# Kernel tuning notes

Measured on AMD Instinct MI355X. Metric: run time of the kernel, lower is better.

Reference implementation:

```python
import jax, jax.numpy as jnp
import numpy as np

DX, DZ, DT = 10.0, 10.0, 1.0e-3
NX, NZ = 512, 512
NSTEPS, NREC = 512, 128
DT2 = DT * DT
INV_DXDZ = 1.0 / (DX * DZ)


def setup_inputs() -> dict:
    key = jax.random.key(0)
    k1, k2, k3, k4 = jax.random.split(key, 4)
    # velocity in [1500, 2500] m/s -> CFL stable with dt=1e-3, dx=dz=10
    velocity_model = 1500.0 + 1000.0 * jax.random.uniform(k1, (NX, NZ), dtype=jnp.float32)
    source = jax.random.normal(k2, (NSTEPS,), dtype=jnp.float32)
    rec_x = jax.random.randint(k3, (NREC,), 0, NX)
    rec_z = jax.random.randint(k4, (NREC,), 0, NZ)
    return {
        "velocity_model": velocity_model,
        "source": source,
        "src_x": 256,
        "src_z": 8,
        "rec_x": rec_x,
        "rec_z": rec_z,
    }


def _laplacian(p):
    # 3x3 cross stencil with zero padding, scaled by 1/(dx*dz) -- identical to
    # F.conv2d(p, [[0,1,0],[1,-4,1],[0,1,0]]/(dx*dz), padding=1)
    pp = jnp.pad(p, 1)
    return (pp[:-2, 1:-1] + pp[2:, 1:-1] + pp[1:-1, :-2] + pp[1:-1, 2:] - 4.0 * p) * INV_DXDZ


def reference(velocity_model, source, src_x, src_z, rec_x, rec_z):
    v2_dt2 = velocity_model * velocity_model * DT2  # [nx, nz]

    def step(carry, s_t):
        p, p_old = carry
        p_new = 2.0 * p - p_old + v2_dt2 * _laplacian(p)
        p_new = p_new.at[src_x, src_z].add(s_t * DT2)
        return (p_new, p), p_new[rec_x, rec_z]  # gather all receivers at once

    p0 = jnp.zeros((NX, NZ), dtype=velocity_model.dtype)
    _, recs = jax.lax.scan(step, (p0, p0), source)  # recs: [n_steps, n_rec]
    return recs.T  # seismogram: [n_rec, n_steps]
```

## Files before the change

### kernel.cpp

```cpp
#include <hip/hip_runtime.h>


#define NXd 512
#define NZd 512
#define NSTEPSd 512
#define NRECd 128
#define DT2f 1.0e-6f
#define INVf 1.0e-2f
#define TBk 16
#define TIk 32
#define EXTk 64
#define NTILEk 16
#define PADk 16
#define PWk 544
#define LROWS 66
#define NROUNDS (NSTEPSd / TBk)

__device__ __forceinline__ float dpp_shr1(float x) {
    int v = __builtin_amdgcn_update_dpp(0, __builtin_bit_cast(int, x),
                                        0x138, 0xF, 0xF, false);
    return __builtin_bit_cast(float, v);
}
__device__ __forceinline__ float dpp_shl1(float x) {
    int v = __builtin_amdgcn_update_dpp(0, __builtin_bit_cast(int, x),
                                        0x130, 0xF, 0xF, false);
    return __builtin_bit_cast(float, v);
}

__device__ __forceinline__ float2 ldg_f2(const float2* p) {
    unsigned long long v = __hip_atomic_load(
        (const unsigned long long*)p, __ATOMIC_RELAXED, __HIP_MEMORY_SCOPE_AGENT);
    return __builtin_bit_cast(float2, v);
}
__device__ __forceinline__ void stg_f2(float2* p, float2 x) {
    __hip_atomic_store((unsigned long long*)p,
                       __builtin_bit_cast(unsigned long long, x),
                       __ATOMIC_RELAXED, __HIP_MEMORY_SCOPE_AGENT);
}

__global__ __launch_bounds__(1024) void fdtd_persist(
    const float* __restrict__ vel, const float* __restrict__ source,
    const int* __restrict__ src_x, const int* __restrict__ src_z,
    const int* __restrict__ rec_x, const int* __restrict__ rec_z,
    float2* __restrict__ PA, float2* __restrict__ PB,
    float* __restrict__ out, unsigned* __restrict__ done)
{
    __shared__ float sb[2][LROWS * EXTk];

    const int tid = threadIdx.x;
    const int w   = tid >> 6;
    const int ez  = tid & 63;
    const int bx = blockIdx.x, by = blockIdx.y;
    const int gx0 = by * TIk;
    const int gz0 = bx * TIk;
    const int ox = gx0 - TBk, oz = gz0 - TBk;
    const int myid = (by * NTILEk + bx) * 32;

    for (int i = tid; i < 34 * 34; i += 1024) {
        const int p = (by * 34 + i / 34) * PWk + (bx * 34 + i % 34);
        stg_f2(&PA[p], make_float2(0.f, 0.f));
        stg_f2(&PB[p], make_float2(0.f, 0.f));
    }

    bool rOwn = false; int rIdx = 0;
    if (tid < NRECd) {
        const int rx = rec_x[tid], rz = rec_z[tid];
        rOwn = (rx >= gx0 && rx < gx0 + TIk && rz >= gz0 && rz < gz0 + TIk);
        rIdx = (rx - ox + 1) * EXTk + (rz - oz);
        if (rOwn) {
            float4* o4 = (float4*)&out[tid * NSTEPSd];
            #pragma unroll
            for (int j = 0; j < NSTEPSd / 4; ++j) o4[j] = make_float4(0.f, 0.f, 0.f, 0.f);
        }
    }

    float rV2i[4];
    {
        const int fz = oz + ez;
        #pragma unroll
        for (int i = 0; i < 4; ++i) {
            const int fx = ox + 4 * w + i;
            float v2 = 0.f;
            if (fx >= 0 && fx < NXd && fz >= 0 && fz < NZd) {
                float v = vel[fx * NZd + fz];
                v2 = v * v * (DT2f * INVf);
            }
            rV2i[i] = v2;
        }
    }

    if (w == 0) {
        sb[0][ez] = 0.f;
        sb[0][(LROWS - 1) * EXTk + ez] = 0.f;
        sb[1][ez] = 0.f;
        sb[1][(LROWS - 1) * EXTk + ez] = 0.f;
    }

    const int sx = *src_x, sz = *src_z;
    const int exs = sx - ox, ezs = sz - oz;
    const bool srcHere = (exs >= 0 && exs < EXTk && ezs >= 0 && ezs < EXTk) &&
                         (tid == (((exs >> 2) << 6) | ezs));

    const int dxm = max(0, max(ox - sx, sx - (ox + EXTk - 1)));
    const int dzm = max(0, max(oz - sz, sz - (oz + EXTk - 1)));
    const int dman = dxm + dzm;
    const int kAct = dman <= (TBk + 1) ? 0 : (dman - (TBk + 1) + TBk - 1) / TBk;

    int nb = myid;
    if (tid < 8) {
        const int d = (tid < 4) ? tid : tid + 1;
        const int ny = min(NTILEk - 1, max(0, by + d / 3 - 1));
        const int nx = min(NTILEk - 1, max(0, bx + d % 3 - 1));
        nb = (ny * NTILEk + nx) * 32;
    }

    const int pbase = (gx0 + 4 * w) * PWk + gz0 + ez;
    const int fbase = 4 * w * EXTk + ez;

    __syncthreads();
    if (tid == 0)
        __hip_atomic_store(&done[myid], (unsigned)(kAct + 1),
                           __ATOMIC_RELAXED, __HIP_MEMORY_SCOPE_AGENT);

    for (int k = kAct; k < NROUNDS; ++k) {
        const int t0 = TBk * k;

        if (tid < 8) {
            const unsigned tgt = (unsigned)(k + 1);
            while (__hip_atomic_load(&done[nb], __ATOMIC_RELAXED,
                                     __HIP_MEMORY_SCOPE_AGENT) < tgt)
                __builtin_amdgcn_s_sleep(1);
        }
        __syncthreads();

        float2* __restrict__ Pin  = (k & 1) ? PB : PA;
        float2* __restrict__ Pout = (k & 1) ? PA : PB;

        float2 co[4];
        #pragma unroll
        for (int i = 0; i < 4; ++i) co[i] = ldg_f2(&Pin[pbase + i * PWk]);

        float rCur[4], rOld[4];
        #pragma unroll
        for (int i = 0; i < 4; ++i) {
            rCur[i] = co[i].x; rOld[i] = co[i].y;
            sb[0][(4 * w + 1 + i) * EXTk + ez] = rCur[i];
        }

        float sv[TBk];
        if (srcHere) {
            #pragma unroll
            for (int s = 0; s < TBk; ++s) sv[s] = source[t0 + s] * DT2f;
        }

        __syncthreads();

        float rv[TBk];
        #pragma unroll
        for (int s = 0; s < TBk; ++s) {
            const float* cur = sb[s & 1];
            float* nxt = sb[(s & 1) ^ 1];
            const float up0 = cur[fbase];
            const float dn3 = cur[fbase + 5 * EXTk];
            float nv[4];
            #pragma unroll
            for (int i = 0; i < 4; ++i) {
                const float up = (i == 0) ? up0 : rCur[i - 1];
                const float dn = (i == 3) ? dn3 : rCur[i + 1];
                const float lf = dpp_shr1(rCur[i]);
                const float rt = dpp_shl1(rCur[i]);
                const float sum = (up + dn) + (lf + rt);
                const float t4 = __builtin_fmaf(-4.0f, rCur[i], sum);
                const float pm = __builtin_fmaf(2.0f, rCur[i], -rOld[i]);
                nv[i] = __builtin_fmaf(rV2i[i], t4, pm);
            }
            #pragma unroll
            for (int i = 0; i < 4; ++i) {
                rOld[i] = rCur[i];
                rCur[i] = nv[i];
                nxt[fbase + (1 + i) * EXTk] = nv[i];
            }
            if (srcHere) {
                #pragma unroll
                for (int i = 0; i < 4; ++i) {
                    if (i == (exs & 3)) {
                        rCur[i] += sv[s];
                        nxt[(exs + 1) * EXTk + ezs] = rCur[i];
                    }
                }
            }
            __syncthreads();
            if (rOwn) rv[s] = nxt[rIdx];
        }

        if (w >= 4 && w < 12 && ez >= TBk && ez < EXTk - TBk) {
            #pragma unroll
            for (int i = 0; i < 4; ++i)
                stg_f2(&Pout[pbase + i * PWk], make_float2(rCur[i], rOld[i]));
        }

        if (rOwn) {
            #pragma unroll
            for (int s = 0; s < TBk; ++s)
                out[tid * NSTEPSd + t0 + s] = rv[s];
        }

        __syncthreads();
        if (tid == 0)
            __hip_atomic_store(&done[myid], (unsigned)(k + 2),
                               __ATOMIC_RELAXED, __HIP_MEMORY_SCOPE_AGENT);
    }
}

extern "C" void kernel_launch(void* const* d_in, const int* in_sizes, int n_in,
                              void* d_out, int out_size, void* d_ws, size_t ws_size,
                              hipStream_t stream) {
    const float* vel    = (const float*)d_in[0];
    const float* source = (const float*)d_in[1];
    const int*   src_x  = (const int*)d_in[2];
    const int*   src_z  = (const int*)d_in[3];
    const int*   rec_x  = (const int*)d_in[4];
    const int*   rec_z  = (const int*)d_in[5];
    float* out = (float*)d_out;

    const size_t FP = (size_t)PWk * PWk;
    float2* PA = (float2*)d_ws;
    float2* PB = PA + FP;
    unsigned* DONE = (unsigned*)(PB + FP);

    hipMemsetAsync(DONE, 0, (size_t)NTILEk * NTILEk * 32 * sizeof(unsigned), stream);

    void* args[] = {(void*)&vel, (void*)&source, (void*)&src_x, (void*)&src_z,
                    (void*)&rec_x, (void*)&rec_z, (void*)&PA, (void*)&PB,
                    (void*)&out, (void*)&DONE};
    hipLaunchCooperativeKernel((void*)fdtd_persist, dim3(NTILEk, NTILEk),
                               dim3(1024), args, 0, stream);
}
```

Baseline: 340.0 us.

## Compute two timesteps per LDS exchange with redundant halo rows to halve barriers

Each wave now reads two halo rows on each side (stored as float2 cur/old pairs) and computes two timesteps per group, recomputing the extra halo rows redundantly. This halves the number of __syncthreads and LDS exchanges per round, from 16 to 8. In exchange each group adds about 50% more stencil arithmetic, wider LDS traffic (float2) and more registers. Source injection and receiver sampling are adapted to handle the pair of steps.

```diff
diff --git a/kernel.cpp b/kernel.cpp
--- a/kernel.cpp
+++ b/kernel.cpp
@@ -13,8 +13,9 @@
 #define NTILEk 16
 #define PADk 16
 #define PWk 544
-#define LROWS 66
+#define LROWS 68
 #define NROUNDS (NSTEPSd / TBk)
+#define NGRP 8
 
 __device__ __forceinline__ float dpp_shr1(float x) {
     int v = __builtin_amdgcn_update_dpp(0, __builtin_bit_cast(int, x),
@@ -45,7 +46,7 @@
     float2* __restrict__ PA, float2* __restrict__ PB,
     float* __restrict__ out, unsigned* __restrict__ done)
 {
-    __shared__ float sb[2][LROWS * EXTk];
+    __shared__ float2 sb[2][LROWS * EXTk];
 
     const int tid = threadIdx.x;
     const int w   = tid >> 6;
@@ -66,7 +67,7 @@
     if (tid < NRECd) {
         const int rx = rec_x[tid], rz = rec_z[tid];
         rOwn = (rx >= gx0 && rx < gx0 + TIk && rz >= gz0 && rz < gz0 + TIk);
-        rIdx = (rx - ox + 1) * EXTk + (rz - oz);
+        rIdx = (rx - ox + 2) * EXTk + (rz - oz);
         if (rOwn) {
             float4* o4 = (float4*)&out[tid * NSTEPSd];
             #pragma unroll
@@ -74,32 +75,35 @@
         }
     }
 
-    float rV2i[4];
+    float rV2x[6];
     {
         const int fz = oz + ez;
         #pragma unroll
-        for (int i = 0; i < 4; ++i) {
-            const int fx = ox + 4 * w + i;
+        for (int j = 0; j < 6; ++j) {
+            const int fx = ox + 4 * w - 1 + j;
             float v2 = 0.f;
             if (fx >= 0 && fx < NXd && fz >= 0 && fz < NZd) {
                 float v = vel[fx * NZd + fz];
                 v2 = v * v * (DT2f * INVf);
             }
-            rV2i[i] = v2;
+            rV2x[j] = v2;
         }
     }
 
     if (w == 0) {
-        sb[0][ez] = 0.f;
-        sb[0][(LROWS - 1) * EXTk + ez] = 0.f;
-        sb[1][ez] = 0.f;
-        sb[1][(LROWS - 1) * EXTk + ez] = 0.f;
+        #pragma unroll
+        for (int b = 0; b < 2; ++b) {
+            sb[b][0 * EXTk + ez]  = make_float2(0.f, 0.f);
+            sb[b][1 * EXTk + ez]  = make_float2(0.f, 0.f);
+            sb[b][66 * EXTk + ez] = make_float2(0.f, 0.f);
+            sb[b][67 * EXTk + ez] = make_float2(0.f, 0.f);
+        }
     }
 
     const int sx = *src_x, sz = *src_z;
     const int exs = sx - ox, ezs = sz - oz;
-    const bool srcHere = (exs >= 0 && exs < EXTk && ezs >= 0 && ezs < EXTk) &&
-                         (tid == (((exs >> 2) << 6) | ezs));
+    const int jA0 = exs - (4 * w - 1);
+    const bool svTouch = (ez == ezs) && (jA0 >= 0) && (jA0 < 6);
 
     const int dxm = max(0, max(ox - sx, sx - (ox + EXTk - 1)));
     const int dzm = max(0, max(oz - sz, sz - (oz + EXTk - 1)));
@@ -115,7 +119,7 @@
     }
 
     const int pbase = (gx0 + 4 * w) * PWk + gz0 + ez;
-    const int fbase = 4 * w * EXTk + ez;
+    const int rd0 = (4 * w) * EXTk + ez;
 
     __syncthreads();
     if (tid == 0)
@@ -144,11 +148,11 @@
         #pragma unroll
         for (int i = 0; i < 4; ++i) {
             rCur[i] = co[i].x; rOld[i] = co[i].y;
-            sb[0][(4 * w + 1 + i) * EXTk + ez] = rCur[i];
+            sb[0][(4 * w + 2 + i) * EXTk + ez] = co[i];
         }
 
         float sv[TBk];
-        if (srcHere) {
+        if (svTouch) {
             #pragma unroll
             for (int s = 0; s < TBk; ++s) sv[s] = source[t0 + s] * DT2f;
         }
@@ -157,40 +161,53 @@
 
         float rv[TBk];
         #pragma unroll
-        for (int s = 0; s < TBk; ++s) {
-            const float* cur = sb[s & 1];
-            float* nxt = sb[(s & 1) ^ 1];
-            const float up0 = cur[fbase];
-            const float dn3 = cur[fbase + 5 * EXTk];
-            float nv[4];
+        for (int g = 0; g < NGRP; ++g) {
+            const float2* cur = sb[g & 1];
+            float2* nxt = sb[(g & 1) ^ 1];
+            const float2 h0 = cur[rd0];
+            const float2 h1 = cur[rd0 + EXTk];
+            const float2 h4 = cur[rd0 + 6 * EXTk];
+            const float2 h5 = cur[rd0 + 7 * EXTk];
+            const float curv[8] = {h0.x, h1.x, rCur[0], rCur[1],
+                                   rCur[2], rCur[3], h4.x, h5.x};
+            const float oldA[6] = {h1.y, rOld[0], rOld[1],
+                                   rOld[2], rOld[3], h4.y};
+            float cA[6];
+            #pragma unroll
+            for (int j = 0; j < 6; ++j) {
+                const float c = curv[j + 1];
+                const float sum = (curv[j] + curv[j + 2]) +
+                                  (dpp_shr1(c) + dpp_shl1(c));
+                cA[j] = __builtin_fmaf(rV2x[j], __builtin_fmaf(-4.0f, c, sum),
+                                       __builtin_fmaf(2.0f, c, -oldA[j]));
+            }
+            #pragma unroll
+            for (int j = 0; j < 6; ++j)
+                if (j == jA0 && svTouch) cA[j] += sv[2 * g];
+            float cB[4];
             #pragma unroll
             for (int i = 0; i < 4; ++i) {
-                const float up = (i == 0) ? up0 : rCur[i - 1];
-                const float dn = (i == 3) ? dn3 : rCur[i + 1];
-                const float lf = dpp_shr1(rCur[i]);
-                const float rt = dpp_shl1(rCur[i]);
-                const float sum = (up + dn) + (lf + rt);
-                const float t4 = __builtin_fmaf(-4.0f, rCur[i], sum);
-                const float pm = __builtin_fmaf(2.0f, rCur[i], -rOld[i]);
-                nv[i] = __builtin_fmaf(rV2i[i], t4, pm);
-            }
+                const float c = cA[i + 1];
+                const float sum = (cA[i] + cA[i + 2]) +
+                                  (dpp_shr1(c) + dpp_shl1(c));
+                cB[i] = __builtin_fmaf(rV2x[i + 1], __builtin_fmaf(-4.0f, c, sum),
+                                       __builtin_fmaf(2.0f, c, -rCur[i]));
+            }
+            #pragma unroll
+            for (int i = 0; i < 4; ++i)
+                if (i + 1 == jA0 && svTouch) cB[i] += sv[2 * g + 1];
             #pragma unroll
             for (int i = 0; i < 4; ++i) {
-                rOld[i] = rCur[i];
-                rCur[i] = nv[i];
-                nxt[fbase + (1 + i) * EXTk] = nv[i];
-            }
-            if (srcHere) {
-                #pragma unroll
-                for (int i = 0; i < 4; ++i) {
-                    if (i == (exs & 3)) {
-                        rCur[i] += sv[s];
-                        nxt[(exs + 1) * EXTk + ezs] = rCur[i];
-                    }
-                }
+                rOld[i] = cA[i + 1];
+                rCur[i] = cB[i];
+                nxt[(4 * w + 2 + i) * EXTk + ez] = make_float2(cB[i], cA[i + 1]);
             }
             __syncthreads();
-            if (rOwn) rv[s] = nxt[rIdx];
+            if (rOwn) {
+                const float2 rr = nxt[rIdx];
+                rv[2 * g]     = rr.y;
+                rv[2 * g + 1] = rr.x;
+            }
         }
 
         if (w >= 4 && w < 12 && ez >= TBk && ez < EXTk - TBk) {
```

Result: slower. 382.5 us (+12.5%).

## Poll neighbor flags per wave and drop LDS staging barriers at round start

Applied to the files above, without the earlier changes.

Every wavefront now spins on the eight neighbor-tile done flags itself, so the block-wide barrier after polling goes away. The initial LDS write of the tile plus its barrier is also removed: step 0 takes its vertical halo directly from global memory, and the workspace is shifted by one padded row so the row above the tile stays in bounds. The tile's done flag is now published before the receiver samples are written to the output, and the polling sleep grows longer when a neighbor is more than one round behind. Together these shorten the inter-tile dependency chain per time block, in exchange for more global polling traffic and subtler memory-ordering assumptions.

```diff
diff --git a/kernel.cpp b/kernel.cpp
--- a/kernel.cpp
+++ b/kernel.cpp
@@ -32,6 +32,11 @@
         (const unsigned long long*)p, __ATOMIC_RELAXED, __HIP_MEMORY_SCOPE_AGENT);
     return __builtin_bit_cast(float2, v);
 }
+__device__ __forceinline__ float ldg_f1(const float* p) {
+    unsigned v = __hip_atomic_load(
+        (const unsigned*)p, __ATOMIC_RELAXED, __HIP_MEMORY_SCOPE_AGENT);
+    return __builtin_bit_cast(float, v);
+}
 __device__ __forceinline__ void stg_f2(float2* p, float2 x) {
     __hip_atomic_store((unsigned long long*)p,
                        __builtin_bit_cast(unsigned long long, x),
@@ -106,9 +111,10 @@
     const int dman = dxm + dzm;
     const int kAct = dman <= (TBk + 1) ? 0 : (dman - (TBk + 1) + TBk - 1) / TBk;
 
+    const int lane = tid & 63;
     int nb = myid;
-    if (tid < 8) {
-        const int d = (tid < 4) ? tid : tid + 1;
+    if (lane < 8) {
+        const int d = (lane < 4) ? lane : lane + 1;
         const int ny = min(NTILEk - 1, max(0, by + d / 3 - 1));
         const int nx = min(NTILEk - 1, max(0, bx + d % 3 - 1));
         nb = (ny * NTILEk + nx) * 32;
@@ -125,13 +131,16 @@
     for (int k = kAct; k < NROUNDS; ++k) {
         const int t0 = TBk * k;
 
-        if (tid < 8) {
+        if (lane < 8) {
             const unsigned tgt = (unsigned)(k + 1);
-            while (__hip_atomic_load(&done[nb], __ATOMIC_RELAXED,
-                                     __HIP_MEMORY_SCOPE_AGENT) < tgt)
-                __builtin_amdgcn_s_sleep(1);
-        }
-        __syncthreads();
+            for (;;) {
+                unsigned seen = __hip_atomic_load(&done[nb], __ATOMIC_RELAXED,
+                                                  __HIP_MEMORY_SCOPE_AGENT);
+                if (seen >= tgt) break;
+                if (seen + 1 < tgt) __builtin_amdgcn_s_sleep(16);
+                else                __builtin_amdgcn_s_sleep(1);
+            }
+        }
 
         float2* __restrict__ Pin  = (k & 1) ? PB : PA;
         float2* __restrict__ Pout = (k & 1) ? PA : PB;
@@ -139,29 +148,26 @@
         float2 co[4];
         #pragma unroll
         for (int i = 0; i < 4; ++i) co[i] = ldg_f2(&Pin[pbase + i * PWk]);
+        const float huG = ldg_f1((const float*)&Pin[pbase - PWk]);
+        const float hdG = ldg_f1((const float*)&Pin[pbase + 4 * PWk]);
 
         float rCur[4], rOld[4];
         #pragma unroll
-        for (int i = 0; i < 4; ++i) {
-            rCur[i] = co[i].x; rOld[i] = co[i].y;
-            sb[0][(4 * w + 1 + i) * EXTk + ez] = rCur[i];
-        }
+        for (int i = 0; i < 4; ++i) { rCur[i] = co[i].x; rOld[i] = co[i].y; }
 
         float sv[TBk];
         if (srcHere) {
             #pragma unroll
             for (int s = 0; s < TBk; ++s) sv[s] = source[t0 + s] * DT2f;
         }
-
-        __syncthreads();
 
         float rv[TBk];
         #pragma unroll
         for (int s = 0; s < TBk; ++s) {
             const float* cur = sb[s & 1];
             float* nxt = sb[(s & 1) ^ 1];
-            const float up0 = cur[fbase];
-            const float dn3 = cur[fbase + 5 * EXTk];
+            const float up0 = (s == 0) ? huG : cur[fbase];
+            const float dn3 = (s == 0) ? hdG : cur[fbase + 5 * EXTk];
             float nv[4];
             #pragma unroll
             for (int i = 0; i < 4; ++i) {
@@ -199,16 +205,16 @@
                 stg_f2(&Pout[pbase + i * PWk], make_float2(rCur[i], rOld[i]));
         }
 
-        if (rOwn) {
-            #pragma unroll
-            for (int s = 0; s < TBk; ++s)
-                out[tid * NSTEPSd + t0 + s] = rv[s];
-        }
-
         __syncthreads();
         if (tid == 0)
             __hip_atomic_store(&done[myid], (unsigned)(k + 2),
                                __ATOMIC_RELAXED, __HIP_MEMORY_SCOPE_AGENT);
+
+        if (rOwn) {
+            #pragma unroll
+            for (int s = 0; s < TBk; ++s)
+                out[tid * NSTEPSd + t0 + s] = rv[s];
+        }
     }
 }
 
@@ -224,9 +230,10 @@
     float* out = (float*)d_out;
 
     const size_t FP = (size_t)PWk * PWk;
-    float2* PA = (float2*)d_ws;
+    float2* base = (float2*)d_ws;
+    float2* PA = base + PWk;
     float2* PB = PA + FP;
-    unsigned* DONE = (unsigned*)(PB + FP);
+    unsigned* DONE = (unsigned*)(PB + FP + PWk);
 
     hipMemsetAsync(DONE, 0, (size_t)NTILEk * NTILEk * 32 * sizeof(unsigned), stream);
 
```

After: 340.4 us, median of 2. No clear change (+0.1%).
